# Kernel tuning notes

Measured on AMD Instinct MI355X. Metric: run time of the kernel, lower is better.

The kernel has to match this reference:

```python
import jax, jax.numpy as jnp
import numpy as np

K = 8192   # num_embeddings
D = 256    # embedding_dim


def setup_inputs() -> dict:
    key = jax.random.key(0)
    k1, k2 = jax.random.split(key)
    inputs = jax.random.normal(k1, (8, 4096, D), dtype=jnp.float32)
    # torch init: uniform_(-1/num_embeddings, 1/num_embeddings)
    embeddings_weight = jax.random.uniform(
        k2, (K, D), dtype=jnp.float32, minval=-1.0 / K, maxval=1.0 / K
    )
    return {"inputs": inputs, "embeddings_weight": embeddings_weight}


def reference(inputs, embeddings_weight):
    in_shape = inputs.shape
    flat = inputs.reshape(-1, D)                      # [N, D]
    distances = (
        jnp.sum(flat * flat, axis=1, keepdims=True)   # [N, 1]
        + jnp.sum(embeddings_weight * embeddings_weight, axis=1)  # [K]
        - 2.0 * jnp.matmul(flat, embeddings_weight.T)             # [N, K]
    )
    encoding_indices = jnp.argmin(distances, axis=1)  # [N] int
    # one-hot @ W is mathematically a row gather of W
    quantized = jnp.take(embeddings_weight, encoding_indices, axis=0).reshape(in_shape)
    return quantized, encoding_indices
```

## Files before the change

kernel.cpp:

```cpp
#include <hip/hip_runtime.h>
#include <cfloat>


#define DDIM 256

typedef int   i32x8  __attribute__((ext_vector_type(8)));
typedef float f32x16 __attribute__((ext_vector_type(16)));

__global__ __launch_bounds__(256) void vq_prep_w(
    const float* __restrict__ w, float* __restrict__ wn,
    unsigned char* __restrict__ wb8) {
    __shared__ float rows[32 * 260];
    const int tid = threadIdx.x;
    const int r0 = blockIdx.x * 32;

    for (int idx = tid; idx < 32 * 64; idx += 256) {
        int r = idx >> 6, c4 = idx & 63;
        *(float4*)&rows[r * 260 + c4 * 4] =
            *(const float4*)(w + (size_t)(r0 + r) * DDIM + c4 * 4);
    }
    __syncthreads();
    {
        const int row = (tid >> 6) * 8 + ((tid & 63) >> 3), j = tid & 7;
        const float* a = &rows[row * 260];
        float half[2];
#pragma unroll
        for (int h = 0; h < 2; ++h) {
            const float* b = a + h * 128 + j;
            float r = __fmul_rn(b[0], b[0]);
#pragma unroll
            for (int t = 1; t < 16; ++t)
                r = __fadd_rn(r, __fmul_rn(b[8 * t], b[8 * t]));
            float p = __fadd_rn(r, __shfl_xor(r, 1, 64));
            p = __fadd_rn(p, __shfl_xor(p, 2, 64));
            p = __fadd_rn(p, __shfl_xor(p, 4, 64));
            half[h] = p;
        }
        if (j == 0) wn[r0 + row] = __fadd_rn(half[0], half[1]);
    }
    for (int idx = tid; idx < 32 * 16; idx += 256) {
        int r = idx >> 4, s = idx & 15;
        const float* p = &rows[r * 260 + s * 16];
        unsigned q[4];
#pragma unroll
        for (int m = 0; m < 4; ++m) {
            unsigned v = (unsigned)__builtin_amdgcn_cvt_pk_fp8_f32(
                p[m * 4 + 0] * -8192.f, p[m * 4 + 1] * -8192.f, 0, false);
            v = (unsigned)__builtin_amdgcn_cvt_pk_fp8_f32(
                p[m * 4 + 2] * -8192.f, p[m * 4 + 3] * -8192.f, (int)v, true);
            q[m] = v;
        }
        *(uint4*)(wb8 + (size_t)(r0 + r) * DDIM + s * 16) =
            make_uint4(q[0], q[1], q[2], q[3]);
    }
}


#define VWAIT(n) do { \
    asm volatile("s_waitcnt vmcnt(" #n ")" ::: "memory"); \
    __builtin_amdgcn_sched_barrier(0); \
  } while (0)

#define INIT128(C) { _Pragma("unroll") for (int r_ = 0; r_ < 16; ++r_) (C)[r_] = 128.0f; }

#define SEL16(P, rt, pkt) { \
    const unsigned colv_ = (unsigned)((pkt) * 128 + bcol); \
    _Pragma("unroll") for (int r_ = 0; r_ < 16; ++r_) { \
        unsigned key_ = (__float_as_uint((P)[r_]) & 0xFFFFE000u) | colv_; \
        unsigned a0_ = s0[rt][r_]; \
        unsigned mx_ = key_ > a0_ ? key_ : a0_; \
        s1[rt][r_] = mx_ < s1[rt][r_] ? mx_ : s1[rt][r_]; \
        s0[rt][r_] = key_ < a0_ ? key_ : a0_; \
    } }

__global__ __launch_bounds__(256, 2) void vq_score(
    const float* __restrict__ x, const unsigned char* __restrict__ wb8,
    unsigned* __restrict__ cand) {
    __shared__ __align__(16) unsigned char Ws[2][32768];
    const int tid = threadIdx.x;
    const int wave = tid >> 6, lane = tid & 63;
    const int h = lane >> 5, c32 = lane & 31;
    const int rowBase = blockIdx.x * 64;
    const unsigned char* wsb = (const unsigned char*)&Ws[0][0];

    i32x8 af[2][4];
#pragma unroll
    for (int rt = 0; rt < 2; ++rt) {
        const float* xr = x + (size_t)(rowBase + rt * 32 + c32) * DDIM;
#pragma unroll
        for (int ks = 0; ks < 4; ++ks) {
            const float4* p = (const float4*)(xr + ks * 64 + h * 32);
            union { int d[8]; i32x8 v; } u;
#pragma unroll
            for (int m = 0; m < 8; ++m) {
                float4 f = p[m];
                unsigned v = (unsigned)__builtin_amdgcn_cvt_pk_fp8_f32(
                    f.x, f.y, 0, false);
                v = (unsigned)__builtin_amdgcn_cvt_pk_fp8_f32(
                    f.z, f.w, (int)v, true);
                u.d[m] = (int)v;
            }
            af[rt][ks] = u.v;
        }
    }
    asm volatile("s_waitcnt vmcnt(0)" ::: "memory");

    unsigned sOfs[8], ldsOfs[8];
#pragma unroll
    for (int i = 0; i < 8; ++i) {
        int slot = wave * 8 + i;
        int col  = slot * 4 + (lane >> 4);
        int gsrc = (lane & 15) ^ (col & 15);
        sOfs[i]   = (unsigned)(col * 256 + gsrc * 16);
        ldsOfs[i] = (unsigned)(slot * 1024);
    }
    auto stage = [&](int kt, unsigned tgl) {
        const unsigned char* g = wb8 + (size_t)kt * 32768;
#pragma unroll
        for (int i = 0; i < 8; ++i)
            __builtin_amdgcn_global_load_lds(
                (const __attribute__((address_space(1))) unsigned int*)(g + sOfs[i]),
                (__attribute__((address_space(3))) unsigned int*)(
                    &Ws[0][0] + tgl + ldsOfs[i]),
                16, 0, 0);
    };

    const int bcol = wave * 32 + c32, cs = bcol & 15;
    int bofs[4][2];
#pragma unroll
    for (int ks = 0; ks < 4; ++ks) {
        int gb = ks * 4 + h * 2;
        bofs[ks][0] = bcol * 256 + ((gb)     ^ cs) * 16;
        bofs[ks][1] = bcol * 256 + ((gb + 1) ^ cs) * 16;
    }

    unsigned s0[2][16], s1[2][16];
#pragma unroll
    for (int a = 0; a < 2; ++a)
#pragma unroll
        for (int r = 0; r < 16; ++r) { s0[a][r] = 0xFFFFFFFFu; s1[a][r] = 0xFFFFFFFFu; }

    f32x16 acc0, acc1;

    stage(0, 0);

    for (int kt = 0; kt < 63; ++kt) {
        const unsigned tgl = (unsigned)(kt & 1) << 15;
        stage(kt + 1, tgl ^ 32768u);
        INIT128(acc0); INIT128(acc1);
        VWAIT(8);
        __builtin_amdgcn_s_setprio(1);
#pragma unroll
        for (int ks = 0; ks < 4; ++ks) {
            union { uint4 q[2]; i32x8 v; } b_;
            b_.q[0] = *(const uint4*)(wsb + tgl + bofs[ks][0]);
            b_.q[1] = *(const uint4*)(wsb + tgl + bofs[ks][1]);
            acc0 = __builtin_amdgcn_mfma_scale_f32_32x32x64_f8f6f4(
                af[0][ks], b_.v, acc0, 0, 0, 0, 0x7F7F7F7F, 0, 0x7F7F7F7F);
            acc1 = __builtin_amdgcn_mfma_scale_f32_32x32x64_f8f6f4(
                af[1][ks], b_.v, acc1, 0, 0, 0, 0x7F7F7F7F, 0, 0x7F7F7F7F);
        }
        __builtin_amdgcn_s_setprio(0);
        SEL16(acc0, 0, kt);
        SEL16(acc1, 1, kt);
    }
    {
        INIT128(acc0); INIT128(acc1);
        VWAIT(0);
        __builtin_amdgcn_s_setprio(1);
#pragma unroll
        for (int ks = 0; ks < 4; ++ks) {
            union { uint4 q[2]; i32x8 v; } b_;
            b_.q[0] = *(const uint4*)(wsb + 32768 + bofs[ks][0]);
            b_.q[1] = *(const uint4*)(wsb + 32768 + bofs[ks][1]);
            acc0 = __builtin_amdgcn_mfma_scale_f32_32x32x64_f8f6f4(
                af[0][ks], b_.v, acc0, 0, 0, 0, 0x7F7F7F7F, 0, 0x7F7F7F7F);
            acc1 = __builtin_amdgcn_mfma_scale_f32_32x32x64_f8f6f4(
                af[1][ks], b_.v, acc1, 0, 0, 0, 0x7F7F7F7F, 0, 0x7F7F7F7F);
        }
        __builtin_amdgcn_s_setprio(0);
        SEL16(acc0, 0, 63);
        SEL16(acc1, 1, 63);
    }

    __syncthreads();
    unsigned* ms = (unsigned*)Ws;
#pragma unroll
    for (int rt = 0; rt < 2; ++rt)
#pragma unroll
        for (int r = 0; r < 16; ++r) {
            int rloc = rt * 32 + (r & 3) + 8 * (r >> 2) + 4 * h;
            *(uint2*)&ms[rloc * 256 + bcol * 2] = make_uint2(s0[rt][r], s1[rt][r]);
        }
    __syncthreads();
    if (tid < 64) {
        const uint4* rowk = (const uint4*)(ms + tid * 256);
        unsigned best[8];
#pragma unroll
        for (int i = 0; i < 8; ++i) best[i] = 0xFFFFFFFFu;
        for (int i = 0; i < 64; ++i) {
            uint4 qv = rowk[(i + tid) & 63];
            unsigned kk[4] = {qv.x, qv.y, qv.z, qv.w};
#pragma unroll
            for (int e = 0; e < 4; ++e) {
                unsigned key = kk[e];
                if (key < best[7]) {
                    best[7] = key;
#pragma unroll
                    for (int j = 7; j > 0; --j)
                        if (best[j] < best[j - 1]) {
                            unsigned t = best[j]; best[j] = best[j - 1]; best[j - 1] = t;
                        }
                }
            }
        }
        unsigned* out = cand + (size_t)(rowBase + tid) * 8;
#pragma unroll
        for (int i = 0; i < 8; ++i) out[i] = best[i];
    }
}

__global__ __launch_bounds__(256) void vq_rescore_write(
    const float* __restrict__ x, const float* __restrict__ w,
    const float* __restrict__ wn, const unsigned* __restrict__ cand,
    float* __restrict__ outq, float* __restrict__ outi) {
    __shared__ int winners[32];
    const int tid = threadIdx.x;
    const int lr = tid >> 3, cc = tid & 7;
    const int row = blockIdx.x * 32 + lr;

    int k = (int)(cand[(size_t)row * 8 + cc] & 0x1FFFu);
    const float* xr = x + (size_t)row * DDIM;
    const float* wr = w + (size_t)k * DDIM;
    float dot = 0.f;
    float half[2];
#pragma unroll
    for (int hh = 0; hh < 2; ++hh) {
        float r[8];
#pragma unroll
        for (int t = 0; t < 16; ++t) {
            const int d = hh * 128 + t * 8;
            float4 xa = *(const float4*)(xr + d);
            float4 xb = *(const float4*)(xr + d + 4);
            float4 wa = *(const float4*)(wr + d);
            float4 wb = *(const float4*)(wr + d + 4);
            dot = __fmaf_rn(xa.x, wa.x, dot); dot = __fmaf_rn(xa.y, wa.y, dot);
            dot = __fmaf_rn(xa.z, wa.z, dot); dot = __fmaf_rn(xa.w, wa.w, dot);
            dot = __fmaf_rn(xb.x, wb.x, dot); dot = __fmaf_rn(xb.y, wb.y, dot);
            dot = __fmaf_rn(xb.z, wb.z, dot); dot = __fmaf_rn(xb.w, wb.w, dot);
            if (t == 0) {
                r[0] = __fmul_rn(xa.x, xa.x); r[1] = __fmul_rn(xa.y, xa.y);
                r[2] = __fmul_rn(xa.z, xa.z); r[3] = __fmul_rn(xa.w, xa.w);
                r[4] = __fmul_rn(xb.x, xb.x); r[5] = __fmul_rn(xb.y, xb.y);
                r[6] = __fmul_rn(xb.z, xb.z); r[7] = __fmul_rn(xb.w, xb.w);
            } else {
                r[0] = __fadd_rn(r[0], __fmul_rn(xa.x, xa.x));
                r[1] = __fadd_rn(r[1], __fmul_rn(xa.y, xa.y));
                r[2] = __fadd_rn(r[2], __fmul_rn(xa.z, xa.z));
                r[3] = __fadd_rn(r[3], __fmul_rn(xa.w, xa.w));
                r[4] = __fadd_rn(r[4], __fmul_rn(xb.x, xb.x));
                r[5] = __fadd_rn(r[5], __fmul_rn(xb.y, xb.y));
                r[6] = __fadd_rn(r[6], __fmul_rn(xb.w == xb.w ? xb.z : xb.z, xb.z));
                r[7] = __fadd_rn(r[7], __fmul_rn(xb.w, xb.w));
            }
        }
        half[hh] = __fadd_rn(__fadd_rn(__fadd_rn(r[0], r[1]), __fadd_rn(r[2], r[3])),
                             __fadd_rn(__fadd_rn(r[4], r[5]), __fadd_rn(r[6], r[7])));
    }
    float x2v = __fadd_rn(half[0], half[1]);
    float dv = __fsub_rn(__fadd_rn(x2v, wn[k]), __fmul_rn(2.0f, dot));
#pragma unroll
    for (int m = 1; m < 8; m <<= 1) {
        float od = __shfl_xor(dv, m, 64);
        int   ok = __shfl_xor(k,  m, 64);
        if (od < dv || (od == dv && ok < k)) { dv = od; k = ok; }
    }
    if (cc == 0) winners[lr] = k;
    __syncthreads();
    if (tid < 32) outi[blockIdx.x * 32 + tid] = (float)winners[tid];
    for (int u = tid; u < 32 * 64; u += 256) {
        int r = u >> 6, c4 = u & 63;
        *reinterpret_cast<float4*>(outq + (size_t)(blockIdx.x * 32 + r) * DDIM + c4 * 4) =
            *reinterpret_cast<const float4*>(w + (size_t)winners[r] * DDIM + c4 * 4);
    }
}

extern "C" void kernel_launch(void* const* d_in, const int* in_sizes, int n_in,
                              void* d_out, int out_size, void* d_ws, size_t ws_size,
                              hipStream_t stream) {
    const float* x = (const float*)d_in[0];
    const float* w = (const float*)d_in[1];
    const int N = in_sizes[0] / DDIM;
    const int K = in_sizes[1] / DDIM;
    float* outq = (float*)d_out;
    float* outi = outq + (size_t)N * DDIM;

    unsigned char* wb8 = (unsigned char*)d_ws;
    float* wn = (float*)(wb8 + (size_t)K * DDIM);
    unsigned* cand = (unsigned*)(wn + K);

    hipLaunchKernelGGL(vq_prep_w, dim3(K / 32), dim3(256), 0, stream, w, wn, wb8);
    hipLaunchKernelGGL(vq_score, dim3(N / 64), dim3(256), 0, stream, x, wb8, cand);
    hipLaunchKernelGGL(vq_rescore_write, dim3(N / 32), dim3(256), 0, stream,
                       x, w, wn, cand, outq, outi);
}
```

Measured before the change: 249.9 us.

## Software-pipeline top-2 selection and LDS B loads under MFMA chain

The per-tile top-2 key selection is deferred by one tile: keys from the previous tile are packed into a register buffer and merged in chunks interleaved between the MFMA instructions of the next tile. The LDS B-fragment loads are also double-buffered so the next k-step's fragment loads ahead of the current MFMA. The aim is to hide the VALU selection work and LDS latency behind matrix-core execution. The cost is 32 extra registers per thread, which may pressure occupancy at 2 blocks/CU. The initial dummy pk values of all-ones leave the first merge harmless.

```diff
diff --git a/kernel.cpp b/kernel.cpp
--- a/kernel.cpp
+++ b/kernel.cpp
@@ -63,15 +63,35 @@
 
 #define INIT128(C) { _Pragma("unroll") for (int r_ = 0; r_ < 16; ++r_) (C)[r_] = 128.0f; }
 
-#define SEL16(P, rt, pkt) { \
+#define SELCH(ks) { \
+    _Pragma("unroll") for (int j_ = 0; j_ < 4; ++j_) { \
+        const int r_ = (ks) * 4 + j_; \
+        _Pragma("unroll") for (int rt_ = 0; rt_ < 2; ++rt_) { \
+            unsigned key_ = pk[rt_][r_]; \
+            unsigned a0_ = s0[rt_][r_]; \
+            unsigned mx_ = key_ > a0_ ? key_ : a0_; \
+            s1[rt_][r_] = mx_ < s1[rt_][r_] ? mx_ : s1[rt_][r_]; \
+            s0[rt_][r_] = key_ < a0_ ? key_ : a0_; \
+        } } }
+
+#define KEYX(pkt) { \
     const unsigned colv_ = (unsigned)((pkt) * 128 + bcol); \
     _Pragma("unroll") for (int r_ = 0; r_ < 16; ++r_) { \
-        unsigned key_ = (__float_as_uint((P)[r_]) & 0xFFFFE000u) | colv_; \
-        unsigned a0_ = s0[rt][r_]; \
-        unsigned mx_ = key_ > a0_ ? key_ : a0_; \
-        s1[rt][r_] = mx_ < s1[rt][r_] ? mx_ : s1[rt][r_]; \
-        s0[rt][r_] = key_ < a0_ ? key_ : a0_; \
+        pk[0][r_] = (__float_as_uint(acc0[r_]) & 0xFFFFE000u) | colv_; \
+        pk[1][r_] = (__float_as_uint(acc1[r_]) & 0xFFFFE000u) | colv_; \
     } }
+
+#define STEP(ks, BC, BN, NK, TGL) do { \
+    if (NK) { \
+        BN.q[0] = *(const uint4*)(wsb + (TGL) + bofs[(ks) + 1][0]); \
+        BN.q[1] = *(const uint4*)(wsb + (TGL) + bofs[(ks) + 1][1]); \
+    } \
+    acc0 = __builtin_amdgcn_mfma_scale_f32_32x32x64_f8f6f4( \
+        af[0][ks], BC.v, acc0, 0, 0, 0, 0x7F7F7F7F, 0, 0x7F7F7F7F); \
+    acc1 = __builtin_amdgcn_mfma_scale_f32_32x32x64_f8f6f4( \
+        af[1][ks], BC.v, acc1, 0, 0, 0, 0x7F7F7F7F, 0, 0x7F7F7F7F); \
+    SELCH(ks); \
+  } while (0)
 
 __global__ __launch_bounds__(256, 2) void vq_score(
     const float* __restrict__ x, const unsigned char* __restrict__ wb8,
@@ -134,13 +154,17 @@
         bofs[ks][1] = bcol * 256 + ((gb + 1) ^ cs) * 16;
     }
 
-    unsigned s0[2][16], s1[2][16];
+    unsigned s0[2][16], s1[2][16], pk[2][16];
 #pragma unroll
     for (int a = 0; a < 2; ++a)
 #pragma unroll
-        for (int r = 0; r < 16; ++r) { s0[a][r] = 0xFFFFFFFFu; s1[a][r] = 0xFFFFFFFFu; }
+        for (int r = 0; r < 16; ++r) {
+            s0[a][r] = 0xFFFFFFFFu; s1[a][r] = 0xFFFFFFFFu; pk[a][r] = 0xFFFFFFFFu;
+        }
 
     f32x16 acc0, acc1;
+    union Bu { uint4 q[2]; i32x8 v; };
+    Bu bA, bB;
 
     stage(0, 0);
 
@@ -149,38 +173,29 @@
         stage(kt + 1, tgl ^ 32768u);
         INIT128(acc0); INIT128(acc1);
         VWAIT(8);
+        bA.q[0] = *(const uint4*)(wsb + tgl + bofs[0][0]);
+        bA.q[1] = *(const uint4*)(wsb + tgl + bofs[0][1]);
         __builtin_amdgcn_s_setprio(1);
-#pragma unroll
-        for (int ks = 0; ks < 4; ++ks) {
-            union { uint4 q[2]; i32x8 v; } b_;
-            b_.q[0] = *(const uint4*)(wsb + tgl + bofs[ks][0]);
-            b_.q[1] = *(const uint4*)(wsb + tgl + bofs[ks][1]);
-            acc0 = __builtin_amdgcn_mfma_scale_f32_32x32x64_f8f6f4(
-                af[0][ks], b_.v, acc0, 0, 0, 0, 0x7F7F7F7F, 0, 0x7F7F7F7F);
-            acc1 = __builtin_amdgcn_mfma_scale_f32_32x32x64_f8f6f4(
-                af[1][ks], b_.v, acc1, 0, 0, 0, 0x7F7F7F7F, 0, 0x7F7F7F7F);
-        }
+        STEP(0, bA, bB, 1, tgl);
+        STEP(1, bB, bA, 1, tgl);
+        STEP(2, bA, bB, 1, tgl);
+        STEP(3, bB, bA, 0, tgl);
         __builtin_amdgcn_s_setprio(0);
-        SEL16(acc0, 0, kt);
-        SEL16(acc1, 1, kt);
+        KEYX(kt);
     }
     {
         INIT128(acc0); INIT128(acc1);
         VWAIT(0);
+        bA.q[0] = *(const uint4*)(wsb + 32768 + bofs[0][0]);
+        bA.q[1] = *(const uint4*)(wsb + 32768 + bofs[0][1]);
         __builtin_amdgcn_s_setprio(1);
-#pragma unroll
-        for (int ks = 0; ks < 4; ++ks) {
-            union { uint4 q[2]; i32x8 v; } b_;
-            b_.q[0] = *(const uint4*)(wsb + 32768 + bofs[ks][0]);
-            b_.q[1] = *(const uint4*)(wsb + 32768 + bofs[ks][1]);
-            acc0 = __builtin_amdgcn_mfma_scale_f32_32x32x64_f8f6f4(
-                af[0][ks], b_.v, acc0, 0, 0, 0, 0x7F7F7F7F, 0, 0x7F7F7F7F);
-            acc1 = __builtin_amdgcn_mfma_scale_f32_32x32x64_f8f6f4(
-                af[1][ks], b_.v, acc1, 0, 0, 0, 0x7F7F7F7F, 0, 0x7F7F7F7F);
-        }
+        STEP(0, bA, bB, 1, 32768u);
+        STEP(1, bB, bA, 1, 32768u);
+        STEP(2, bA, bB, 1, 32768u);
+        STEP(3, bB, bA, 0, 32768u);
         __builtin_amdgcn_s_setprio(0);
-        SEL16(acc0, 0, 63);
-        SEL16(acc1, 1, 63);
+        KEYX(63);
+        SELCH(0); SELCH(1); SELCH(2); SELCH(3);
     }
 
     __syncthreads();
```

Result: no change. 251.0 us (+0.5%).
